# Kernel tuning notes

Measured on AMD Instinct MI355X. Metric: run time of the kernel, lower is better.

Reference implementation:

```python
import jax, jax.numpy as jnp
import numpy as np

HIDDEN = 2560
N_HEADS = 32
HEAD_DIM = HIDDEN // N_HEADS  # 80
ROPE_PCT = 0.25
ROT = int(HEAD_DIM * ROPE_PCT)  # 20
THETA = 10000.0


def setup_inputs() -> dict:
    key = jax.random.key(0)
    ks = jax.random.split(key, 6)
    B, S = 2, 2048
    hidden_states = jax.random.normal(ks[0], (B, S, HIDDEN), dtype=jnp.float32)
    attention_mask = jnp.ones((B, S), dtype=jnp.float32)  # unused in no-cache path
    position_ids = jnp.tile(jnp.arange(S, dtype=jnp.int32)[None, :], (B, 1))
    scale = 1.0 / np.sqrt(HIDDEN)
    Wq = jax.random.normal(ks[1], (HIDDEN, HIDDEN), dtype=jnp.float32) * scale
    Wk = jax.random.normal(ks[2], (HIDDEN, HIDDEN), dtype=jnp.float32) * scale
    Wv = jax.random.normal(ks[3], (HIDDEN, HIDDEN), dtype=jnp.float32) * scale
    Wo = jax.random.normal(ks[4], (HIDDEN, HIDDEN), dtype=jnp.float32) * scale
    return {"hidden_states": hidden_states, "attention_mask": attention_mask,
            "position_ids": position_ids, "Wq": Wq, "Wk": Wk, "Wv": Wv, "Wo": Wo}


def _rotate_half(x):
    x1, x2 = jnp.split(x, 2, axis=-1)
    return jnp.concatenate([-x2, x1], axis=-1)


def _rope_cos_sin(position_ids, dtype):
    # inv_freq over rotary dims
    inv_freq = 1.0 / (THETA ** (jnp.arange(0, ROT, 2, dtype=jnp.float32) / ROT))
    pos = position_ids.astype(jnp.float32)  # [B,S]
    freqs = pos[..., None] * inv_freq[None, None, :]  # [B,S,ROT/2]
    emb = jnp.concatenate([freqs, freqs], axis=-1)    # [B,S,ROT]
    cos = jnp.cos(emb)[:, None, :, :].astype(dtype)   # [B,1,S,ROT]
    sin = jnp.sin(emb)[:, None, :, :].astype(dtype)
    return cos, sin


def reference(hidden_states, attention_mask, position_ids, Wq, Wk, Wv, Wo):
    B, S, H = hidden_states.shape
    dtype = hidden_states.dtype
    # projections: [B,S,H] -> [B,nh,S,hd]
    def split_heads(x):
        return x.reshape(B, S, N_HEADS, HEAD_DIM).transpose(0, 2, 1, 3)
    q = split_heads(hidden_states @ Wq)
    k = split_heads(hidden_states @ Wk)
    v = split_heads(hidden_states @ Wv)

    # partial RoPE on first ROT dims
    cos, sin = _rope_cos_sin(position_ids, dtype)
    q_rot, q_pass = q[..., :ROT], q[..., ROT:]
    k_rot, k_pass = k[..., :ROT], k[..., ROT:]
    q_rot = q_rot * cos + _rotate_half(q_rot) * sin
    k_rot = k_rot * cos + _rotate_half(k_rot) * sin
    q = jnp.concatenate([q_rot, q_pass], axis=-1)
    k = jnp.concatenate([k_rot, k_pass], axis=-1)

    # causal attention (no KV cache -> is_causal=True SDPA path)
    scale = 1.0 / np.sqrt(HEAD_DIM)
    scores = jnp.einsum("bhqd,bhkd->bhqk", q, k) * scale
    causal = jnp.tril(jnp.ones((S, S), dtype=bool))
    scores = jnp.where(causal[None, None, :, :], scores, jnp.finfo(jnp.float32).min)
    probs = jax.nn.softmax(scores.astype(jnp.float32), axis=-1).astype(dtype)
    attn = jnp.einsum("bhqk,bhkd->bhqd", probs, v)
    attn = attn.transpose(0, 2, 1, 3).reshape(B, S, H)
    return attn @ Wo
```

## Files before the change

### kernel.cpp

```cpp
#include <hip/hip_runtime.h>
#include <stdint.h>

typedef unsigned short u16;
typedef __bf16 bf16x8 __attribute__((ext_vector_type(8)));
typedef float floatx4 __attribute__((ext_vector_type(4)));

#define HIDDEN 2560
#define NHEADS 32
#define HD 80
#define SEQ 2048
#define BATCH 2
#define MROWS (BATCH*SEQ)
#define QB 128

__device__ __forceinline__ float bf2f(uint32_t bits) {
    return __uint_as_float(bits << 16);
}
__device__ __forceinline__ u16 f2bf_bits(float f) {
    uint32_t x = __float_as_uint(f);
    uint32_t r = (x + 0x7fffu + ((x >> 16) & 1u)) >> 16;
    return (u16)r;
}
__device__ __forceinline__ floatx4 mk4(float x) {
    return (floatx4){x, x, x, x};
}
__device__ __forceinline__ floatx4 max4(floatx4 a, floatx4 b) {
    floatx4 r;
#pragma unroll
    for (int i = 0; i < 4; i++) r[i] = fmaxf(a[i], b[i]);
    return r;
}
__device__ __forceinline__ floatx4 exp4(floatx4 a) {
    floatx4 r;
#pragma unroll
    for (int i = 0; i < 4; i++) r[i] = __expf(a[i]);
    return r;
}
template <int N>
__device__ __forceinline__ floatx4 ror16_4(floatx4 v) {
    floatx4 r;
#pragma unroll
    for (int i = 0; i < 4; i++)
        r[i] = __int_as_float(__builtin_amdgcn_update_dpp(
            0, __float_as_int(v[i]), 0x120 + N, 0xF, 0xF, true));
    return r;
}
__device__ __forceinline__ floatx4 redmax16(floatx4 v) {
    v = max4(v, ror16_4<1>(v));
    v = max4(v, ror16_4<2>(v));
    v = max4(v, ror16_4<4>(v));
    v = max4(v, ror16_4<8>(v));
    return v;
}
__device__ __forceinline__ floatx4 redsum16(floatx4 v) {
    v = v + ror16_4<1>(v);
    v = v + ror16_4<2>(v);
    v = v + ror16_4<4>(v);
    v = v + ror16_4<8>(v);
    return v;
}
__device__ __forceinline__ void gload16(const u16* g, u16* l) {
    __builtin_amdgcn_global_load_lds(
        (const __attribute__((address_space(1))) uint32_t*)g,
        (__attribute__((address_space(3))) uint32_t*)l, 16, 0, 0);
}

__global__ __launch_bounds__(256) void split_x(const float* __restrict__ in,
                                               u16* __restrict__ hi,
                                               u16* __restrict__ lo) {
    size_t i4 = (size_t)blockIdx.x * 256 + threadIdx.x;
    float4 v = ((const float4*)in)[i4];
    float f[4] = {v.x, v.y, v.z, v.w};
    u16 h[4], l[4];
#pragma unroll
    for (int j = 0; j < 4; j++) {
        h[j] = f2bf_bits(f[j]);
        l[j] = f2bf_bits(f[j] - bf2f(h[j]));
    }
    ((uint2*)hi)[i4] = *(uint2*)h;
    ((uint2*)lo)[i4] = *(uint2*)l;
}

__global__ __launch_bounds__(256) void split_wt(const float* __restrict__ in,
                                                u16* __restrict__ outh,
                                                u16* __restrict__ outl) {
    __shared__ float t[64][65];
    int k0 = blockIdx.x * 64;
    int n0 = blockIdx.y * 64;
    int tid = threadIdx.x;
    int rr = tid >> 4;
    int c4 = (tid & 15) * 4;
#pragma unroll
    for (int it = 0; it < 4; it++) {
        int row = it * 16 + rr;
        float4 v = *(const float4*)&in[(size_t)(k0 + row) * HIDDEN + n0 + c4];
        t[row][c4 + 0] = v.x; t[row][c4 + 1] = v.y;
        t[row][c4 + 2] = v.z; t[row][c4 + 3] = v.w;
    }
    __syncthreads();
#pragma unroll
    for (int it = 0; it < 4; it++) {
        int row = it * 16 + rr;
        float f[4] = { t[c4 + 0][row], t[c4 + 1][row], t[c4 + 2][row], t[c4 + 3][row] };
        u16 h[4], l[4];
#pragma unroll
        for (int j = 0; j < 4; j++) {
            h[j] = f2bf_bits(f[j]);
            l[j] = f2bf_bits(f[j] - bf2f(h[j]));
        }
        size_t o = (size_t)(n0 + row) * HIDDEN + k0 + c4;
        *(uint2*)&outh[o] = *(uint2*)h;
        *(uint2*)&outl[o] = *(uint2*)l;
    }
}

__global__ __launch_bounds__(256) void gemm_bt2(const u16* __restrict__ Ah,
                                                const u16* __restrict__ Al,
                                                const u16* __restrict__ Bh,
                                                const u16* __restrict__ Bl,
                                                float* __restrict__ C) {
    __shared__ u16 lAh[128 * 32];
    __shared__ u16 lAl[128 * 32];
    __shared__ u16 lBh[128 * 32];
    __shared__ u16 lBl[128 * 32];
    const int K = HIDDEN;
    int tid  = threadIdx.x;
    int lane = tid & 63;
    int wave = tid >> 6;
    int wr = wave >> 1, wc = wave & 1;
    int m0 = blockIdx.y * 128, n0 = blockIdx.x * 128;
    int lr = lane & 15, lq = lane >> 4;

    int srow = wave * 32 + (lane >> 2);
    int scol = ((lane & 3) ^ ((lane >> 3) & 3)) * 8;
    const u16* gAh = Ah + (size_t)(m0 + srow) * K + scol;
    const u16* gAl = Al + (size_t)(m0 + srow) * K + scol;
    const u16* gBh = Bh + (size_t)(n0 + srow) * K + scol;
    const u16* gBl = Bl + (size_t)(n0 + srow) * K + scol;
    const size_t q1 = (size_t)16 * K;
    u16* dAh = &lAh[(wave * 32) * 32];
    u16* dAl = &lAl[(wave * 32) * 32];
    u16* dBh = &lBh[(wave * 32) * 32];
    u16* dBl = &lBl[(wave * 32) * 32];

    floatx4 acc[4][4];
#pragma unroll
    for (int i = 0; i < 4; i++)
#pragma unroll
        for (int j = 0; j < 4; j++)
            acc[i][j] = mk4(0.f);

    int swz = (lr >> 1) & 3;
    int rsl = (lq ^ swz) * 8;

    for (int k0 = 0; k0 < K; k0 += 32) {
        gload16(gAh + k0, dAh);  gload16(gAh + q1 + k0, dAh + 16 * 32);
        gload16(gAl + k0, dAl);  gload16(gAl + q1 + k0, dAl + 16 * 32);
        gload16(gBh + k0, dBh);  gload16(gBh + q1 + k0, dBh + 16 * 32);
        gload16(gBl + k0, dBl);  gload16(gBl + q1 + k0, dBl + 16 * 32);
        __syncthreads();
        bf16x8 ah[4], al[4], bh[4], bl[4];
#pragma unroll
        for (int i = 0; i < 4; i++) {
            int ra = (wr * 64 + i * 16 + lr) * 32 + rsl;
            int rb = (wc * 64 + i * 16 + lr) * 32 + rsl;
            ah[i] = *(const bf16x8*)&lAh[ra];
            al[i] = *(const bf16x8*)&lAl[ra];
            bh[i] = *(const bf16x8*)&lBh[rb];
            bl[i] = *(const bf16x8*)&lBl[rb];
        }
#pragma unroll
        for (int i = 0; i < 4; i++)
#pragma unroll
            for (int j = 0; j < 4; j++) {
                acc[i][j] = __builtin_amdgcn_mfma_f32_16x16x32_bf16(ah[i], bh[j], acc[i][j], 0, 0, 0);
                acc[i][j] = __builtin_amdgcn_mfma_f32_16x16x32_bf16(ah[i], bl[j], acc[i][j], 0, 0, 0);
                acc[i][j] = __builtin_amdgcn_mfma_f32_16x16x32_bf16(al[i], bh[j], acc[i][j], 0, 0, 0);
            }
        __syncthreads();
    }
#pragma unroll
    for (int i = 0; i < 4; i++) {
        int rowb = m0 + wr * 64 + i * 16 + lq * 4;
#pragma unroll
        for (int j = 0; j < 4; j++) {
            int col = n0 + wc * 64 + j * 16 + lr;
#pragma unroll
            for (int r = 0; r < 4; r++)
                C[(size_t)(rowb + r) * HIDDEN + col] = acc[i][j][r];
        }
    }
}

__global__ __launch_bounds__(256) void rope_k(float* __restrict__ Qb, float* __restrict__ Kb,
                                              const int* __restrict__ pos_ids) {
    int idx = blockIdx.x * 256 + threadIdx.x;
    int row = idx >> 5;
    int h   = idx & 31;
    float pos = (float)pos_ids[row];
    size_t base = (size_t)row * HIDDEN + h * HD;
    float* q = Qb + base;
    float* k = Kb + base;
#pragma unroll
    for (int i = 0; i < 10; i++) {
        float freq = pos * exp2f(-1.3287712379549449f * (float)i);
        float sn, cs;
        sincosf(freq, &sn, &cs);
        float q1 = q[i], q2 = q[i + 10];
        q[i]      = q1 * cs - q2 * sn;
        q[i + 10] = q2 * cs + q1 * sn;
        float k1 = k[i], k2 = k[i + 10];
        k[i]      = k1 * cs - k2 * sn;
        k[i + 10] = k2 * cs + k1 * sn;
    }
}

__global__ __launch_bounds__(256) void vtrans(const float* __restrict__ Vb,
                                              u16* __restrict__ Vth,
                                              u16* __restrict__ Vtl) {
    __shared__ float t[64][81];
    int bh = blockIdx.x; int b = bh >> 5, h = bh & 31;
    int s0 = blockIdx.y * 64;
    int tid = threadIdx.x;
    for (int idx = tid; idx < 64 * 20; idx += 256) {
        int s = idx / 20, c = idx % 20;
        float4 v = *(const float4*)&Vb[(size_t)(b * SEQ + s0 + s) * HIDDEN + h * HD + c * 4];
        t[s][c * 4 + 0] = v.x; t[s][c * 4 + 1] = v.y;
        t[s][c * 4 + 2] = v.z; t[s][c * 4 + 3] = v.w;
    }
    __syncthreads();
    for (int idx = tid; idx < 80 * 8; idx += 256) {
        int d = idx >> 3, sc = idx & 7;
        u16 hh[8], ll[8];
#pragma unroll
        for (int j = 0; j < 8; j++) {
            float f = t[sc * 8 + j][d];
            hh[j] = f2bf_bits(f);
            ll[j] = f2bf_bits(f - bf2f(hh[j]));
        }
        size_t o = ((size_t)bh * HD + d) * SEQ + s0 + sc * 8;
        *(int4*)&Vth[o] = *(int4*)hh;
        *(int4*)&Vtl[o] = *(int4*)ll;
    }
}

__global__ __launch_bounds__(256) void attn_mfma(const u16* __restrict__ Qh_,
                                                 const u16* __restrict__ Ql_,
                                                 const u16* __restrict__ Kh_,
                                                 const u16* __restrict__ Kl_,
                                                 const u16* __restrict__ Vth_,
                                                 const u16* __restrict__ Vtl_,
                                                 u16* __restrict__ Oh_,
                                                 u16* __restrict__ Ol_) {
    __shared__ u16 lds[22784];

    int tid = threadIdx.x;
    int lane = tid & 63, w = tid >> 6;
    int lr = lane & 15, lq = lane >> 4;
    int bh = blockIdx.x; int b = bh >> 5, h = bh & 31;
    int qblk = (gridDim.y - 1) - blockIdx.y;
    int q0 = qblk * QB;
    size_t rowbase = (size_t)b * SEQ;
    size_t hoff = (size_t)h * HD;
    const float SC = 0.11180339887498949f;

    bf16x8 qh[2][2], ql[2][2], qta[2], qtb[2];
#pragma unroll
    for (int round = 0; round < 2; round++) {
        for (int idx = tid; idx < 1280; idx += 256) {
            int buf = idx >= 640; int e = idx - buf * 640;
            int r = e / 10, c = e % 10;
            const u16* src = (buf ? Ql_ : Qh_) +
                (rowbase + q0 + round * 64 + r) * HIDDEN + hoff + c * 8;
            *(int4*)&lds[buf * 6656 + r * 104 + c * 8] = *(const int4*)src;
        }
        __syncthreads();
        if ((w >> 1) == round) {
            int wl = w & 1;
            int tba = (lq >> 1) ? 6656 : 0;
            int tbb = (lq >> 1) ? 0 : 6656;
            int tcol = 64 + (lq & 1) * 8;
#pragma unroll
            for (int rt = 0; rt < 2; rt++) {
                int lrow = wl * 32 + rt * 16 + lr;
#pragma unroll
                for (int c = 0; c < 2; c++) {
                    qh[rt][c] = *(const bf16x8*)&lds[lrow * 104 + c * 32 + lq * 8];
                    ql[rt][c] = *(const bf16x8*)&lds[6656 + lrow * 104 + c * 32 + lq * 8];
                }
                qta[rt] = *(const bf16x8*)&lds[tba + lrow * 104 + tcol];
                qtb[rt] = *(const bf16x8*)&lds[tbb + lrow * 104 + tcol];
            }
        }
        __syncthreads();
    }

    floatx4 acc[2][5];
    floatx4 mrow[2], lsum[2];
#pragma unroll
    for (int rt = 0; rt < 2; rt++) {
        mrow[rt] = mk4(-3.0e38f);
        lsum[rt] = mk4(0.f);
#pragma unroll
        for (int nt = 0; nt < 5; nt++) acc[rt][nt] = mk4(0.f);
    }

    int ntiles = 4 * qblk + 4;
    int qw0 = q0 + w * 32;
    u16* lPw = lds + 20480 + w * 576;

    int k0RowOff = (lane >> 3) * HIDDEN + (((lane & 7) ^ (lane >> 3)) * 8);
    int k1RowOff = (lane >> 1) * HIDDEN + 64 + (lane & 1) * 8;
    int vRowOff  = (lane >> 2) * SEQ + ((((lane & 3) ^ ((lane >> 3) & 3))) * 8);
    const u16* kSrc = (w & 1 ? Kl_ : Kh_) + rowbase * HIDDEN + hoff;
    const u16* vSrc = (w == 3 ? Vtl_ : Vth_) + (size_t)bh * HD * SEQ;

    auto stage = [&](int t, int bsel) {
        int k0 = t * 32;
        u16* B = lds + bsel * 10240;
        if (w < 2) {
            const u16* kb = kSrc + (size_t)k0 * HIDDEN;
            u16* d0 = B + w * 2048;
#pragma unroll
            for (int j = 0; j < 4; j++)
                gload16(kb + (size_t)j * 8 * HIDDEN + k0RowOff, d0 + j * 512);
            gload16(kb + k1RowOff, B + 4096 + w * 512);
        } else {
            const u16* vb = vSrc + k0;
            u16* d0 = B + 5120 + (w == 3 ? 2560 : 0);
#pragma unroll
            for (int j = 0; j < 5; j++)
                gload16(vb + (size_t)j * 16 * SEQ + vRowOff, d0 + j * 512);
        }
    };

    int ks0 = ((lq) ^ (lr & 7)) * 8;
    int ks1 = ((4 + lq) ^ (lr & 7)) * 8;
    int k1off = (lq >> 1) * 512 + (lq & 1) * 8;
    int vsl = (lq ^ ((lr >> 1) & 3)) * 8;

    stage(0, 0);

    for (int t = 0; t < ntiles; t++) {
        int k0 = t * 32;
        __syncthreads();
        if (t + 1 < ntiles) stage(t + 1, (t + 1) & 1);
        u16* B = lds + (t & 1) * 10240;
        if (k0 <= qw0 + 31) {
            u16* bK0h = B;
            u16* bK0l = B + 2048;
            u16* bK1  = B + 4096;
            u16* bVh  = B + 5120;
            u16* bVl  = B + 7680;
            __builtin_amdgcn_s_setprio(1);
            bf16x8 kfh[2][2], kfl[2][2], k1f[2];
#pragma unroll
            for (int st = 0; st < 2; st++) {
                int krow = st * 16 + lr;
                kfh[st][0] = *(const bf16x8*)&bK0h[krow * 64 + ks0];
                kfh[st][1] = *(const bf16x8*)&bK0h[krow * 64 + ks1];
                kfl[st][0] = *(const bf16x8*)&bK0l[krow * 64 + ks0];
                kfl[st][1] = *(const bf16x8*)&bK0l[krow * 64 + ks1];
                k1f[st] = *(const bf16x8*)&bK1[krow * 16 + k1off];
            }
#pragma unroll
            for (int rt = 0; rt < 2; rt++) {
                int qrt0 = qw0 + rt * 16;
                if (k0 > qrt0 + 15) continue;
                floatx4 s[2];
#pragma unroll
                for (int st = 0; st < 2; st++) {
                    floatx4 sv = mk4(0.f);
                    sv = __builtin_amdgcn_mfma_f32_16x16x32_bf16(qh[rt][0], kfh[st][0], sv, 0, 0, 0);
                    sv = __builtin_amdgcn_mfma_f32_16x16x32_bf16(qh[rt][0], kfl[st][0], sv, 0, 0, 0);
                    sv = __builtin_amdgcn_mfma_f32_16x16x32_bf16(ql[rt][0], kfh[st][0], sv, 0, 0, 0);
                    sv = __builtin_amdgcn_mfma_f32_16x16x32_bf16(qh[rt][1], kfh[st][1], sv, 0, 0, 0);
                    sv = __builtin_amdgcn_mfma_f32_16x16x32_bf16(qh[rt][1], kfl[st][1], sv, 0, 0, 0);
                    sv = __builtin_amdgcn_mfma_f32_16x16x32_bf16(ql[rt][1], kfh[st][1], sv, 0, 0, 0);
                    sv = __builtin_amdgcn_mfma_f32_16x16x32_bf16(qta[rt], k1f[st], sv, 0, 0, 0);
                    sv = __builtin_amdgcn_mfma_f32_16x16x32_bf16(qtb[rt], k1f[st], sv, 0, 0, 0);
                    s[st] = sv;
                }
                int qg0 = qrt0 + lq * 4;
                int c0 = k0 + lr, c1 = c0 + 16;
#pragma unroll
                for (int r = 0; r < 4; r++) {
                    s[0][r] = (c0 <= qg0 + r) ? s[0][r] * SC : -3.0e38f;
                    s[1][r] = (c1 <= qg0 + r) ? s[1][r] * SC : -3.0e38f;
                }
                floatx4 rm = redmax16(max4(s[0], s[1]));
                int small = (rm[0] <= mrow[rt][0] + 8.f) & (rm[1] <= mrow[rt][1] + 8.f) &
                            (rm[2] <= mrow[rt][2] + 8.f) & (rm[3] <= mrow[rt][3] + 8.f);
                floatx4 p0, p1;
                if (__all(small)) {
                    p0 = exp4(s[0] - mrow[rt]);
                    p1 = exp4(s[1] - mrow[rt]);
                    lsum[rt] = lsum[rt] + redsum16(p0 + p1);
                } else {
                    floatx4 mnew = max4(mrow[rt], rm);
                    floatx4 alpha = exp4(mrow[rt] - mnew);
                    mrow[rt] = mnew;
                    p0 = exp4(s[0] - mnew);
                    p1 = exp4(s[1] - mnew);
                    lsum[rt] = lsum[rt] * alpha + redsum16(p0 + p1);
#pragma unroll
                    for (int nt = 0; nt < 5; nt++) acc[rt][nt] *= alpha;
                }
#pragma unroll
                for (int r = 0; r < 4; r++) {
                    lPw[(lq * 4 + r) * 36 + lr]      = f2bf_bits(p0[r]);
                    lPw[(lq * 4 + r) * 36 + 16 + lr] = f2bf_bits(p1[r]);
                }
                __builtin_amdgcn_s_waitcnt(0xC07F);
                bf16x8 pa = *(const bf16x8*)&lPw[lr * 36 + lq * 8];
#pragma unroll
                for (int nt = 0; nt < 5; nt++) {
                    bf16x8 vh = *(const bf16x8*)&bVh[(nt * 16 + lr) * 32 + vsl];
                    bf16x8 vl = *(const bf16x8*)&bVl[(nt * 16 + lr) * 32 + vsl];
                    acc[rt][nt] = __builtin_amdgcn_mfma_f32_16x16x32_bf16(pa, vh, acc[rt][nt], 0, 0, 0);
                    acc[rt][nt] = __builtin_amdgcn_mfma_f32_16x16x32_bf16(pa, vl, acc[rt][nt], 0, 0, 0);
                }
            }
            __builtin_amdgcn_s_setprio(0);
        }
    }
#pragma unroll
    for (int rt = 0; rt < 2; rt++) {
        floatx4 inv;
#pragma unroll
        for (int r = 0; r < 4; r++) inv[r] = 1.f / lsum[rt][r];
#pragma unroll
        for (int nt = 0; nt < 5; nt++) {
#pragma unroll
            for (int r = 0; r < 4; r++) {
                float o = acc[rt][nt][r] * inv[r];
                u16 hh = f2bf_bits(o);
                u16 ll = f2bf_bits(o - bf2f(hh));
                size_t row = rowbase + qw0 + rt * 16 + lq * 4 + r;
                Oh_[row * HIDDEN + hoff + nt * 16 + lr] = hh;
                Ol_[row * HIDDEN + hoff + nt * 16 + lr] = ll;
            }
        }
    }
}

extern "C" void kernel_launch(void* const* d_in, const int* in_sizes, int n_in,
                              void* d_out, int out_size, void* d_ws, size_t ws_size,
                              hipStream_t stream) {
    const float* hidden = (const float*)d_in[0];
    const int* pos    = (const int*)d_in[2];
    const float* Wq   = (const float*)d_in[3];
    const float* Wk   = (const float*)d_in[4];
    const float* Wv   = (const float*)d_in[5];
    const float* Wo   = (const float*)d_in[6];

    const size_t NQ = (size_t)MROWS * HIDDEN;
    float* ws = (float*)d_ws;
    float* Qb = ws;
    float* Kb = ws + NQ;
    float* Vb = ws + 2 * NQ;
    u16* Ah  = (u16*)(ws + 3 * NQ);
    u16* Al  = Ah + NQ;
    u16* WTh = Al + NQ;
    u16* WTl = WTh + (size_t)HIDDEN * HIDDEN;
    u16* Vth = Ah;
    u16* Vtl = Al;
    u16* Qh  = (u16*)Vb;
    u16* Ql  = Qh + NQ;
    u16* Kh  = (u16*)Qb;
    u16* Kl  = Kh + NQ;
    u16* Oh  = (u16*)Kb;
    u16* Ol  = Oh + NQ;

    dim3 blk(256);
    dim3 wgrid(HIDDEN / 64, HIDDEN / 64);
    dim3 ggrid(HIDDEN / 128, MROWS / 128);

    split_x<<<dim3(NQ / 1024), blk, 0, stream>>>(hidden, Ah, Al);
    split_wt<<<wgrid, blk, 0, stream>>>(Wq, WTh, WTl);
    gemm_bt2<<<ggrid, blk, 0, stream>>>(Ah, Al, WTh, WTl, Qb);
    split_wt<<<wgrid, blk, 0, stream>>>(Wk, WTh, WTl);
    gemm_bt2<<<ggrid, blk, 0, stream>>>(Ah, Al, WTh, WTl, Kb);
    split_wt<<<wgrid, blk, 0, stream>>>(Wv, WTh, WTl);
    gemm_bt2<<<ggrid, blk, 0, stream>>>(Ah, Al, WTh, WTl, Vb);
    rope_k<<<dim3(MROWS * NHEADS / 256), blk, 0, stream>>>(Qb, Kb, pos);
    vtrans<<<dim3(BATCH * NHEADS, SEQ / 64), blk, 0, stream>>>(Vb, Vth, Vtl);
    split_x<<<dim3(NQ / 1024), blk, 0, stream>>>(Qb, Qh, Ql);
    split_x<<<dim3(NQ / 1024), blk, 0, stream>>>(Kb, Kh, Kl);
    attn_mfma<<<dim3(BATCH * NHEADS, SEQ / QB), blk, 0, stream>>>(Qh, Ql, Kh, Kl,
                                                                  Vth, Vtl, Oh, Ol);
    split_wt<<<wgrid, blk, 0, stream>>>(Wo, WTh, WTl);
    gemm_bt2<<<ggrid, blk, 0, stream>>>(Oh, Ol, WTh, WTl, (float*)d_out);
}
```

Before: 1.330 ms.

## Transpose QK^T MFMA to keep P in registers and drop LDS round-trip

Swaps the MFMA operand order so each lane holds a full score row slice, letting softmax reductions use cross-row shuffles and the P tile convert directly into the PV MFMA operand without writing to LDS. V transpose layout is permuted so the register P ordering matches V columns, and the softmax scale is folded into the Q split. The causal mask is applied only on diagonal tiles, LDS is shrunk and launch bounds request higher occupancy. K fragments are now reloaded per row tile, which increases LDS reads.

```diff
diff --git a/kernel.cpp b/kernel.cpp
--- a/kernel.cpp
+++ b/kernel.cpp
@@ -24,40 +24,11 @@
 __device__ __forceinline__ floatx4 mk4(float x) {
     return (floatx4){x, x, x, x};
 }
-__device__ __forceinline__ floatx4 max4(floatx4 a, floatx4 b) {
-    floatx4 r;
-#pragma unroll
-    for (int i = 0; i < 4; i++) r[i] = fmaxf(a[i], b[i]);
-    return r;
-}
 __device__ __forceinline__ floatx4 exp4(floatx4 a) {
     floatx4 r;
 #pragma unroll
     for (int i = 0; i < 4; i++) r[i] = __expf(a[i]);
     return r;
-}
-template <int N>
-__device__ __forceinline__ floatx4 ror16_4(floatx4 v) {
-    floatx4 r;
-#pragma unroll
-    for (int i = 0; i < 4; i++)
-        r[i] = __int_as_float(__builtin_amdgcn_update_dpp(
-            0, __float_as_int(v[i]), 0x120 + N, 0xF, 0xF, true));
-    return r;
-}
-__device__ __forceinline__ floatx4 redmax16(floatx4 v) {
-    v = max4(v, ror16_4<1>(v));
-    v = max4(v, ror16_4<2>(v));
-    v = max4(v, ror16_4<4>(v));
-    v = max4(v, ror16_4<8>(v));
-    return v;
-}
-__device__ __forceinline__ floatx4 redsum16(floatx4 v) {
-    v = v + ror16_4<1>(v);
-    v = v + ror16_4<2>(v);
-    v = v + ror16_4<4>(v);
-    v = v + ror16_4<8>(v);
-    return v;
 }
 __device__ __forceinline__ void gload16(const u16* g, u16* l) {
     __builtin_amdgcn_global_load_lds(
@@ -67,10 +38,11 @@
 
 __global__ __launch_bounds__(256) void split_x(const float* __restrict__ in,
                                                u16* __restrict__ hi,
-                                               u16* __restrict__ lo) {
+                                               u16* __restrict__ lo,
+                                               float scale) {
     size_t i4 = (size_t)blockIdx.x * 256 + threadIdx.x;
     float4 v = ((const float4*)in)[i4];
-    float f[4] = {v.x, v.y, v.z, v.w};
+    float f[4] = {v.x * scale, v.y * scale, v.z * scale, v.w * scale};
     u16 h[4], l[4];
 #pragma unroll
     for (int j = 0; j < 4; j++) {
@@ -229,22 +201,25 @@
         t[s][c * 4 + 2] = v.z; t[s][c * 4 + 3] = v.w;
     }
     __syncthreads();
-    for (int idx = tid; idx < 80 * 8; idx += 256) {
-        int d = idx >> 3, sc = idx & 7;
-        u16 hh[8], ll[8];
-#pragma unroll
-        for (int j = 0; j < 8; j++) {
-            float f = t[sc * 8 + j][d];
+    for (int idx = tid; idx < 80 * 16; idx += 256) {
+        int d = idx >> 4, ch = idx & 15;
+        int t2 = ch >> 3, e = ch & 7, a = e >> 1, h2 = e & 1;
+        int srck = t2 * 32 + 16 * h2 + 4 * a;
+        int dstc = t2 * 32 + 8 * a + 4 * h2;
+        u16 hh[4], ll[4];
+#pragma unroll
+        for (int j = 0; j < 4; j++) {
+            float f = t[srck + j][d];
             hh[j] = f2bf_bits(f);
             ll[j] = f2bf_bits(f - bf2f(hh[j]));
         }
-        size_t o = ((size_t)bh * HD + d) * SEQ + s0 + sc * 8;
-        *(int4*)&Vth[o] = *(int4*)hh;
-        *(int4*)&Vtl[o] = *(int4*)ll;
-    }
-}
-
-__global__ __launch_bounds__(256) void attn_mfma(const u16* __restrict__ Qh_,
+        size_t o = ((size_t)bh * HD + d) * SEQ + s0 + dstc;
+        *(uint2*)&Vth[o] = *(uint2*)hh;
+        *(uint2*)&Vtl[o] = *(uint2*)ll;
+    }
+}
+
+__global__ __launch_bounds__(256, 4) void attn_mfma(const u16* __restrict__ Qh_,
                                                  const u16* __restrict__ Ql_,
                                                  const u16* __restrict__ Kh_,
                                                  const u16* __restrict__ Kl_,
@@ -252,7 +227,7 @@
                                                  const u16* __restrict__ Vtl_,
                                                  u16* __restrict__ Oh_,
                                                  u16* __restrict__ Ol_) {
-    __shared__ u16 lds[22784];
+    __shared__ u16 lds[20480];
 
     int tid = threadIdx.x;
     int lane = tid & 63, w = tid >> 6;
@@ -262,9 +237,8 @@
     int q0 = qblk * QB;
     size_t rowbase = (size_t)b * SEQ;
     size_t hoff = (size_t)h * HD;
-    const float SC = 0.11180339887498949f;
-
-    bf16x8 qh[2][2], ql[2][2], qta[2], qtb[2];
+
+    bf16x8 qh[2][2], ql[2][2], qta[2];
 #pragma unroll
     for (int round = 0; round < 2; round++) {
         for (int idx = tid; idx < 1280; idx += 256) {
@@ -278,7 +252,6 @@
         if ((w >> 1) == round) {
             int wl = w & 1;
             int tba = (lq >> 1) ? 6656 : 0;
-            int tbb = (lq >> 1) ? 0 : 6656;
             int tcol = 64 + (lq & 1) * 8;
 #pragma unroll
             for (int rt = 0; rt < 2; rt++) {
@@ -289,25 +262,23 @@
                     ql[rt][c] = *(const bf16x8*)&lds[6656 + lrow * 104 + c * 32 + lq * 8];
                 }
                 qta[rt] = *(const bf16x8*)&lds[tba + lrow * 104 + tcol];
-                qtb[rt] = *(const bf16x8*)&lds[tbb + lrow * 104 + tcol];
             }
         }
         __syncthreads();
     }
 
     floatx4 acc[2][5];
-    floatx4 mrow[2], lsum[2];
+    float mrow[2], lsum[2];
 #pragma unroll
     for (int rt = 0; rt < 2; rt++) {
-        mrow[rt] = mk4(-3.0e38f);
-        lsum[rt] = mk4(0.f);
+        mrow[rt] = -3.0e38f;
+        lsum[rt] = 0.f;
 #pragma unroll
         for (int nt = 0; nt < 5; nt++) acc[rt][nt] = mk4(0.f);
     }
 
     int ntiles = 4 * qblk + 4;
     int qw0 = q0 + w * 32;
-    u16* lPw = lds + 20480 + w * 576;
 
     int k0RowOff = (lane >> 3) * HIDDEN + (((lane & 7) ^ (lane >> 3)) * 8);
     int k1RowOff = (lane >> 1) * HIDDEN + 64 + (lane & 1) * 8;
@@ -336,7 +307,8 @@
 
     int ks0 = ((lq) ^ (lr & 7)) * 8;
     int ks1 = ((4 + lq) ^ (lr & 7)) * 8;
-    int k1off = (lq >> 1) * 512 + (lq & 1) * 8;
+    int k1off  = (lq >> 1) * 512 + (lq & 1) * 8;
+    int k1offb = ((lq >> 1) ^ 1) * 512 + (lq & 1) * 8;
     int vsl = (lq ^ ((lr >> 1) & 3)) * 8;
 
     stage(0, 0);
@@ -353,16 +325,6 @@
             u16* bVh  = B + 5120;
             u16* bVl  = B + 7680;
             __builtin_amdgcn_s_setprio(1);
-            bf16x8 kfh[2][2], kfl[2][2], k1f[2];
-#pragma unroll
-            for (int st = 0; st < 2; st++) {
-                int krow = st * 16 + lr;
-                kfh[st][0] = *(const bf16x8*)&bK0h[krow * 64 + ks0];
-                kfh[st][1] = *(const bf16x8*)&bK0h[krow * 64 + ks1];
-                kfl[st][0] = *(const bf16x8*)&bK0l[krow * 64 + ks0];
-                kfl[st][1] = *(const bf16x8*)&bK0l[krow * 64 + ks1];
-                k1f[st] = *(const bf16x8*)&bK1[krow * 16 + k1off];
-            }
 #pragma unroll
             for (int rt = 0; rt < 2; rt++) {
                 int qrt0 = qw0 + rt * 16;
@@ -370,49 +332,63 @@
                 floatx4 s[2];
 #pragma unroll
                 for (int st = 0; st < 2; st++) {
+                    int krow = st * 16 + lr;
+                    bf16x8 kh0 = *(const bf16x8*)&bK0h[krow * 64 + ks0];
+                    bf16x8 kh1 = *(const bf16x8*)&bK0h[krow * 64 + ks1];
+                    bf16x8 kl0 = *(const bf16x8*)&bK0l[krow * 64 + ks0];
+                    bf16x8 kl1 = *(const bf16x8*)&bK0l[krow * 64 + ks1];
+                    bf16x8 k1f  = *(const bf16x8*)&bK1[krow * 16 + k1off];
+                    bf16x8 k1fb = *(const bf16x8*)&bK1[krow * 16 + k1offb];
                     floatx4 sv = mk4(0.f);
-                    sv = __builtin_amdgcn_mfma_f32_16x16x32_bf16(qh[rt][0], kfh[st][0], sv, 0, 0, 0);
-                    sv = __builtin_amdgcn_mfma_f32_16x16x32_bf16(qh[rt][0], kfl[st][0], sv, 0, 0, 0);
-                    sv = __builtin_amdgcn_mfma_f32_16x16x32_bf16(ql[rt][0], kfh[st][0], sv, 0, 0, 0);
-                    sv = __builtin_amdgcn_mfma_f32_16x16x32_bf16(qh[rt][1], kfh[st][1], sv, 0, 0, 0);
-                    sv = __builtin_amdgcn_mfma_f32_16x16x32_bf16(qh[rt][1], kfl[st][1], sv, 0, 0, 0);
-                    sv = __builtin_amdgcn_mfma_f32_16x16x32_bf16(ql[rt][1], kfh[st][1], sv, 0, 0, 0);
-                    sv = __builtin_amdgcn_mfma_f32_16x16x32_bf16(qta[rt], k1f[st], sv, 0, 0, 0);
-                    sv = __builtin_amdgcn_mfma_f32_16x16x32_bf16(qtb[rt], k1f[st], sv, 0, 0, 0);
+                    sv = __builtin_amdgcn_mfma_f32_16x16x32_bf16(kh0, qh[rt][0], sv, 0, 0, 0);
+                    sv = __builtin_amdgcn_mfma_f32_16x16x32_bf16(kl0, qh[rt][0], sv, 0, 0, 0);
+                    sv = __builtin_amdgcn_mfma_f32_16x16x32_bf16(kh0, ql[rt][0], sv, 0, 0, 0);
+                    sv = __builtin_amdgcn_mfma_f32_16x16x32_bf16(kh1, qh[rt][1], sv, 0, 0, 0);
+                    sv = __builtin_amdgcn_mfma_f32_16x16x32_bf16(kl1, qh[rt][1], sv, 0, 0, 0);
+                    sv = __builtin_amdgcn_mfma_f32_16x16x32_bf16(kh1, ql[rt][1], sv, 0, 0, 0);
+                    sv = __builtin_amdgcn_mfma_f32_16x16x32_bf16(k1f,  qta[rt], sv, 0, 0, 0);
+                    sv = __builtin_amdgcn_mfma_f32_16x16x32_bf16(k1fb, qta[rt], sv, 0, 0, 0);
                     s[st] = sv;
                 }
-                int qg0 = qrt0 + lq * 4;
-                int c0 = k0 + lr, c1 = c0 + 16;
-#pragma unroll
-                for (int r = 0; r < 4; r++) {
-                    s[0][r] = (c0 <= qg0 + r) ? s[0][r] * SC : -3.0e38f;
-                    s[1][r] = (c1 <= qg0 + r) ? s[1][r] * SC : -3.0e38f;
+                if (k0 + 31 > qrt0) {
+                    int qmy = qrt0 + lr - k0 - lq * 4;
+#pragma unroll
+                    for (int r = 0; r < 4; r++) {
+                        s[0][r] = (r <= qmy)      ? s[0][r] : -3.0e38f;
+                        s[1][r] = (16 + r <= qmy) ? s[1][r] : -3.0e38f;
+                    }
                 }
-                floatx4 rm = redmax16(max4(s[0], s[1]));
-                int small = (rm[0] <= mrow[rt][0] + 8.f) & (rm[1] <= mrow[rt][1] + 8.f) &
-                            (rm[2] <= mrow[rt][2] + 8.f) & (rm[3] <= mrow[rt][3] + 8.f);
-                floatx4 p0, p1;
-                if (__all(small)) {
-                    p0 = exp4(s[0] - mrow[rt]);
-                    p1 = exp4(s[1] - mrow[rt]);
-                    lsum[rt] = lsum[rt] + redsum16(p0 + p1);
-                } else {
-                    floatx4 mnew = max4(mrow[rt], rm);
-                    floatx4 alpha = exp4(mrow[rt] - mnew);
+                float rm = fmaxf(fmaxf(fmaxf(s[0][0], s[0][1]), fmaxf(s[0][2], s[0][3])),
+                                 fmaxf(fmaxf(s[1][0], s[1][1]), fmaxf(s[1][2], s[1][3])));
+                rm = fmaxf(rm, __shfl_xor(rm, 16));
+                rm = fmaxf(rm, __shfl_xor(rm, 32));
+                int need = rm > mrow[rt] + 8.f;
+                if (__any(need)) {
+                    float mnew = fmaxf(mrow[rt], rm);
+                    float alpha = __expf(mrow[rt] - mnew);
                     mrow[rt] = mnew;
-                    p0 = exp4(s[0] - mnew);
-                    p1 = exp4(s[1] - mnew);
-                    lsum[rt] = lsum[rt] * alpha + redsum16(p0 + p1);
-#pragma unroll
-                    for (int nt = 0; nt < 5; nt++) acc[rt][nt] *= alpha;
+                    lsum[rt] *= alpha;
+                    float at[4];
+#pragma unroll
+                    for (int r = 0; r < 4; r++) at[r] = __shfl(alpha, lq * 4 + r);
+#pragma unroll
+                    for (int nt = 0; nt < 5; nt++)
+#pragma unroll
+                        for (int r = 0; r < 4; r++) acc[rt][nt][r] *= at[r];
                 }
-#pragma unroll
-                for (int r = 0; r < 4; r++) {
-                    lPw[(lq * 4 + r) * 36 + lr]      = f2bf_bits(p0[r]);
-                    lPw[(lq * 4 + r) * 36 + 16 + lr] = f2bf_bits(p1[r]);
-                }
-                __builtin_amdgcn_s_waitcnt(0xC07F);
-                bf16x8 pa = *(const bf16x8*)&lPw[lr * 36 + lq * 8];
+                float m = mrow[rt];
+                floatx4 p0 = exp4(s[0] - mk4(m));
+                floatx4 p1 = exp4(s[1] - mk4(m));
+                floatx4 ps = p0 + p1;
+                float rs = ps[0] + ps[1] + ps[2] + ps[3];
+                rs += __shfl_xor(rs, 16);
+                rs += __shfl_xor(rs, 32);
+                lsum[rt] += rs;
+                bf16x8 pa;
+                pa[0] = (__bf16)p0[0]; pa[1] = (__bf16)p0[1];
+                pa[2] = (__bf16)p0[2]; pa[3] = (__bf16)p0[3];
+                pa[4] = (__bf16)p1[0]; pa[5] = (__bf16)p1[1];
+                pa[6] = (__bf16)p1[2]; pa[7] = (__bf16)p1[3];
 #pragma unroll
                 for (int nt = 0; nt < 5; nt++) {
                     bf16x8 vh = *(const bf16x8*)&bVh[(nt * 16 + lr) * 32 + vsl];
@@ -426,9 +402,10 @@
     }
 #pragma unroll
     for (int rt = 0; rt < 2; rt++) {
-        floatx4 inv;
-#pragma unroll
-        for (int r = 0; r < 4; r++) inv[r] = 1.f / lsum[rt][r];
+        float il = 1.f / lsum[rt];
+        float inv[4];
+#pragma unroll
+        for (int r = 0; r < 4; r++) inv[r] = __shfl(il, lq * 4 + r);
 #pragma unroll
         for (int nt = 0; nt < 5; nt++) {
 #pragma unroll
@@ -472,11 +449,13 @@
     u16* Oh  = (u16*)Kb;
     u16* Ol  = Oh + NQ;
 
+    const float SC = 0.11180339887498949f;
+
     dim3 blk(256);
     dim3 wgrid(HIDDEN / 64, HIDDEN / 64);
     dim3 ggrid(HIDDEN / 128, MROWS / 128);
 
-    split_x<<<dim3(NQ / 1024), blk, 0, stream>>>(hidden, Ah, Al);
+    split_x<<<dim3(NQ / 1024), blk, 0, stream>>>(hidden, Ah, Al, 1.f);
     split_wt<<<wgrid, blk, 0, stream>>>(Wq, WTh, WTl);
     gemm_bt2<<<ggrid, blk, 0, stream>>>(Ah, Al, WTh, WTl, Qb);
     split_wt<<<wgrid, blk, 0, stream>>>(Wk, WTh, WTl);
@@ -485,8 +464,8 @@
     gemm_bt2<<<ggrid, blk, 0, stream>>>(Ah, Al, WTh, WTl, Vb);
     rope_k<<<dim3(MROWS * NHEADS / 256), blk, 0, stream>>>(Qb, Kb, pos);
     vtrans<<<dim3(BATCH * NHEADS, SEQ / 64), blk, 0, stream>>>(Vb, Vth, Vtl);
-    split_x<<<dim3(NQ / 1024), blk, 0, stream>>>(Qb, Qh, Ql);
-    split_x<<<dim3(NQ / 1024), blk, 0, stream>>>(Kb, Kh, Kl);
+    split_x<<<dim3(NQ / 1024), blk, 0, stream>>>(Qb, Qh, Ql, SC);
+    split_x<<<dim3(NQ / 1024), blk, 0, stream>>>(Kb, Kh, Kl, 1.f);
     attn_mfma<<<dim3(BATCH * NHEADS, SEQ / QB), blk, 0, stream>>>(Qh, Ql, Kh, Kl,
                                                                   Vth, Vtl, Oh, Ol);
     split_wt<<<wgrid, blk, 0, stream>>>(Wo, WTh, WTl);
```

New measurement: 1.300 ms. -2.3%, faster.
